# Optimization experiments

Hardware: AMD Instinct MI355X
Metric: run time of the kernel (lower is better)

The kernel has to match this reference:

```python
import jax, jax.numpy as jnp
import numpy as np

N, E = 4096, 131072
D_IN, D_H, H, D_HEAD, D_OUT, L = 768, 256, 4, 64, 128, 2


def setup_inputs() -> dict:
    key = jax.random.key(0)
    ks = jax.random.split(key, 8)
    x = jax.random.normal(ks[0], (N, D_IN), dtype=jnp.float32)
    edge_index = jax.random.randint(ks[1], (2, E), 0, N, dtype=jnp.int64)
    Win = jax.random.normal(ks[2], (D_IN, D_H), dtype=jnp.float32) * 0.02
    bin_ = jnp.zeros((D_H,), dtype=jnp.float32)
    # per-layer, per-head projection weights [L, H, D_H, D_HEAD]
    Wg = jax.random.normal(ks[3], (L, H, D_H, D_HEAD), dtype=jnp.float32) * 0.05
    # per-layer, per-head attention vectors a: [L, H, 2*D_HEAD]
    a = jax.random.normal(ks[4], (L, H, 2 * D_HEAD), dtype=jnp.float32) * 0.05
    Wout = jax.random.normal(ks[5], (D_H, D_OUT), dtype=jnp.float32) * 0.05
    bout = jnp.zeros((D_OUT,), dtype=jnp.float32)
    return {"x": x, "edge_index": edge_index, "Win": Win, "bin_": bin_,
            "Wg": Wg, "a": a, "Wout": Wout, "bout": bout}


def _gat_layer(h, Wl, al, row, col):
    # h: [N, D_H], Wl: [H, D_H, D_HEAD], al: [H, 2*D_HEAD]
    hh = jnp.einsum('ni,hio->hno', h, Wl)          # [H, N, D_HEAD]
    a_src, a_dst = al[:, :D_HEAD], al[:, D_HEAD:]
    s_src = jnp.einsum('hno,ho->hn', hh, a_src)    # [H, N]
    s_dst = jnp.einsum('hno,ho->hn', hh, a_dst)    # [H, N]
    e = jax.nn.leaky_relu(s_src[:, row] + s_dst[:, col], negative_slope=0.2)  # [H, E]
    # dense scatter exactly as the torch module: zeros then assign at (row, col)
    att = jnp.zeros((H, N, N), dtype=h.dtype).at[:, row, col].set(e)
    att = jax.nn.softmax(att, axis=-1)             # dense row softmax (zeros included)
    hp = jnp.einsum('hnm,hmo->hno', att, hh)       # [H, N, D_HEAD]
    return jnp.transpose(hp, (1, 0, 2)).reshape(N, H * D_HEAD)


def reference(x, edge_index, Win, bin_, Wg, a, Wout, bout):
    row, col = edge_index[0], edge_index[1]
    h = jax.nn.relu(x @ Win + bin_)                # input_proj + relu (dropout = eval identity)
    for l in range(L):
        h = jax.nn.relu(_gat_layer(h, Wg[l], a[l], row, col))
    node_embeddings = h @ Wout + bout              # [N, D_OUT]
    return node_embeddings
```

## Files before the change

kernel.cpp:

```cpp
#include <hip/hip_runtime.h>
#include <hip/hip_bf16.h>

#define NNODES 4096
#define NEDGES 131072
#define D_IN   768
#define D_H    256
#define NHEAD  4
#define D_HEAD 64
#define D_OUT  128
#define DEGCAP 192

typedef __attribute__((ext_vector_type(4))) float f32x4;
typedef __attribute__((ext_vector_type(8))) short bf16x8;
typedef __attribute__((ext_vector_type(8))) unsigned short u16x8;

static __device__ __forceinline__ unsigned short f2bf(float f) {
    __hip_bfloat16 h = __float2bfloat16(f);
    return *reinterpret_cast<unsigned short*>(&h);
}
static __device__ __forceinline__ float bf2f(unsigned short u) {
    return __uint_as_float((unsigned)u << 16);
}

#define OFF_H0     (0u)
#define OFF_H1     (4u<<20)
#define OFF_HH     (8u<<20)
#define OFF_SPART  (10u<<20)
#define OFF_SSRC   (OFF_SPART + 131072u)
#define OFF_SDST   (OFF_SSRC + 65536u)
#define OFF_S      (OFF_SDST + 65536u)
#define OFF_WINT   (OFF_S + 1024u)
#define OFF_WGT    (OFF_WINT + 393216u)
#define OFF_WOUTT  (OFF_WGT + 262144u)
#define OFF_BM     (OFF_WOUTT + 65536u)
#define BM_BYTES   ((size_t)NNODES*128u*4u)

__global__ __launch_bounds__(256) void zero_bm(uint4* __restrict__ bm4)
{
    bm4[blockIdx.x*256 + threadIdx.x] = make_uint4(0u,0u,0u,0u);
}

__global__ void edge_bitmap(const int* __restrict__ ei, unsigned* __restrict__ bm)
{
    __shared__ int is64_sh;
    int tid = threadIdx.x;
    if (tid < 64) {
        int v = ei[2*tid + 1];
        unsigned long long ball = __ballot(v == 0);
        if (tid == 0) is64_sh = (ball == ~0ull) ? 1 : 0;
    }
    __syncthreads();
    int is64 = is64_sh;
    int k = blockIdx.x*256 + tid;
    if (k >= NEDGES) return;
    int r = is64 ? ei[2*k]            : ei[k];
    int c = is64 ? ei[2*NEDGES + 2*k] : ei[NEDGES + k];
    r &= (NNODES-1); c &= (NNODES-1);
    atomicOr(&bm[(size_t)r*128 + (c>>5)], 1u << (c & 31));
}

__global__ __launch_bounds__(256) void convert_weights(
    const float* __restrict__ Win, const float* __restrict__ Wg,
    const float* __restrict__ Wout,
    unsigned short* __restrict__ WinT, unsigned short* __restrict__ WgT,
    unsigned short* __restrict__ WoutT)
{
    __shared__ float tile[32][33];
    int mat = blockIdx.y;
    const float* src; unsigned short* dst; int R, Cc;
    if (mat == 0)      { src = Win;                 dst = WinT;                 R = 768; Cc = 256; }
    else if (mat <= 8) { src = Wg + (size_t)(mat-1)*256*64; dst = WgT + (size_t)(mat-1)*64*256; R = 256; Cc = 64; }
    else               { src = Wout;                dst = WoutT;                R = 256; Cc = 128; }
    int tilesC = Cc >> 5;
    int tr = blockIdx.x / tilesC, tc = blockIdx.x % tilesC;
    if (tr*32 >= R) return;
    int ci = threadIdx.x & 31, rq = threadIdx.x >> 5;
    #pragma unroll
    for (int rr = rq; rr < 32; rr += 8)
        tile[rr][ci] = src[(size_t)(tr*32+rr)*Cc + tc*32 + ci];
    __syncthreads();
    int ri = threadIdx.x & 31, cq = threadIdx.x >> 5;
    #pragma unroll
    for (int cc = cq; cc < 32; cc += 8)
        dst[(size_t)(tc*32+cc)*R + tr*32 + ri] = f2bf(tile[ri][cc]);
}

__global__ __launch_bounds__(256) void gemm_mfma(
    const float* __restrict__ A, const unsigned short* __restrict__ BT,
    const float* __restrict__ bias, float* __restrict__ Cf,
    unsigned short* __restrict__ Cb,
    int M, int N, int K, int relu,
    const float* __restrict__ a_l, float* __restrict__ ssrc,
    float* __restrict__ sdst, float* __restrict__ Spart)
{
    __shared__ unsigned short As[32][72];
    __shared__ unsigned short Bs[64][72];
    __shared__ float sredS[4][32], sredD[4][32];
    const int tid = threadIdx.x;
    const int bx = blockIdx.x, by = blockIdx.y;
    const int wc = tid >> 6;
    const int lane = tid & 63;
    const int g = lane >> 4, c = lane & 15;
    const int ar = tid >> 3, ak = (tid & 7) * 8;
    const int bc = tid >> 2, bk = (tid & 3) * 16;
    f32x4 acc0 = {0.f,0.f,0.f,0.f}, acc1 = {0.f,0.f,0.f,0.f};
    const float* Arow = A + (size_t)(by*32 + ar)*K;
    const unsigned short* Brow = BT + (size_t)(bx*64 + bc)*K;

    for (int k0 = 0; k0 < K; k0 += 64) {
        float4 av0 = *(const float4*)&Arow[k0 + ak];
        float4 av1 = *(const float4*)&Arow[k0 + ak + 4];
        u16x8 bv0 = *(const u16x8*)&Brow[k0 + bk];
        u16x8 bv1 = *(const u16x8*)&Brow[k0 + bk + 8];
        ushort4 aw0, aw1;
        aw0.x = f2bf(av0.x); aw0.y = f2bf(av0.y); aw0.z = f2bf(av0.z); aw0.w = f2bf(av0.w);
        aw1.x = f2bf(av1.x); aw1.y = f2bf(av1.y); aw1.z = f2bf(av1.z); aw1.w = f2bf(av1.w);
        *(ushort4*)&As[ar][ak]     = aw0;
        *(ushort4*)&As[ar][ak + 4] = aw1;
        *(u16x8*)&Bs[bc][bk]     = bv0;
        *(u16x8*)&Bs[bc][bk + 8] = bv1;
        __syncthreads();
        bf16x8 b0  = *(bf16x8*)&Bs[wc*16 + c][g*8];
        bf16x8 b1  = *(bf16x8*)&Bs[wc*16 + c][32 + g*8];
        bf16x8 a00 = *(bf16x8*)&As[c][g*8];
        bf16x8 a01 = *(bf16x8*)&As[c][32 + g*8];
        bf16x8 a10 = *(bf16x8*)&As[16 + c][g*8];
        bf16x8 a11 = *(bf16x8*)&As[16 + c][32 + g*8];
        acc0 = __builtin_amdgcn_mfma_f32_16x16x32_bf16(a00, b0, acc0, 0, 0, 0);
        acc0 = __builtin_amdgcn_mfma_f32_16x16x32_bf16(a01, b1, acc0, 0, 0, 0);
        acc1 = __builtin_amdgcn_mfma_f32_16x16x32_bf16(a10, b0, acc1, 0, 0, 0);
        acc1 = __builtin_amdgcn_mfma_f32_16x16x32_bf16(a11, b1, acc1, 0, 0, 0);
        __syncthreads();
    }

    const int col = bx*64 + wc*16 + c;
    float bb = bias ? bias[col] : 0.f;
    #pragma unroll
    for (int t = 0; t < 2; ++t) {
        f32x4 av = t ? acc1 : acc0;
        #pragma unroll
        for (int i = 0; i < 4; ++i) {
            int r = by*32 + t*16 + g*4 + i;
            float v = av[i] + bb;
            if (relu) v = fmaxf(v, 0.f);
            if (Cb) Cb[(size_t)r*N + col] = f2bf(v);
            else    Cf[(size_t)r*N + col] = v;
        }
    }

    if (a_l) {
        int h = bx;
        float as = a_l[h*128 + wc*16 + c];
        float ad = a_l[h*128 + 64 + wc*16 + c];
        float ps[8], pd[8], cs = 0.f;
        #pragma unroll
        for (int t = 0; t < 2; ++t) {
            f32x4 av = t ? acc1 : acc0;
            #pragma unroll
            for (int i = 0; i < 4; ++i) {
                ps[t*4+i] = av[i] * as;
                pd[t*4+i] = av[i] * ad;
                cs += av[i];
            }
        }
        #pragma unroll
        for (int off = 1; off < 16; off <<= 1) {
            #pragma unroll
            for (int j = 0; j < 8; ++j) {
                ps[j] += __shfl_xor(ps[j], off);
                pd[j] += __shfl_xor(pd[j], off);
            }
        }
        if (c == 0) {
            #pragma unroll
            for (int t = 0; t < 2; ++t)
                #pragma unroll
                for (int i = 0; i < 4; ++i) {
                    sredS[wc][t*16 + g*4 + i] = ps[t*4+i];
                    sredD[wc][t*16 + g*4 + i] = pd[t*4+i];
                }
        }
        cs += __shfl_xor(cs, 16);
        cs += __shfl_xor(cs, 32);
        if (g == 0)
            Spart[by*256 + h*64 + wc*16 + c] = cs;
        __syncthreads();
        if (tid < 32) {
            float s1 = sredS[0][tid] + sredS[1][tid] + sredS[2][tid] + sredS[3][tid];
            float s2 = sredD[0][tid] + sredD[1][tid] + sredD[2][tid] + sredD[3][tid];
            int r = by*32 + tid;
            ssrc[r*4 + h] = s1;
            sdst[r*4 + h] = s2;
        }
    }
}

__global__ void colsum2(const float* __restrict__ Spart, float* __restrict__ S)
{
    int j = threadIdx.x;
    float s = 0.f;
    for (int b = 0; b < 128; ++b) s += Spart[b*256 + j];
    S[j] = s;
}

__global__ __launch_bounds__(256) void aggregate_kernel(
    const unsigned* __restrict__ bm,
    const float* __restrict__ ssrc, const float* __restrict__ sdst,
    const unsigned short* __restrict__ hh, const float* __restrict__ S,
    float* __restrict__ hout)
{
    __shared__ int   csr_lds[DEGCAP];
    __shared__ float w_lds[4*DEGCAP];
    __shared__ int   cnt_sh;
    int n = blockIdx.x;
    int tid = threadIdx.x;
    int h = tid >> 6, o = tid & 63;
    const unsigned* brow = bm + (size_t)n*128;

    if (tid < 64) {
        unsigned wA = brow[2*tid], wB = brow[2*tid + 1];
        int cpc = __popc(wA) + __popc(wB);
        int pre = cpc;
        #pragma unroll
        for (int off = 1; off < 64; off <<= 1) {
            int v = __shfl_up(pre, off);
            if (tid >= off) pre += v;
        }
        int excl = pre - cpc;
        int total = __shfl(pre, 63);
        if (total <= DEGCAP) {
            int pos = excl, base = tid*64;
            unsigned w = wA;
            while (w) { int b = __builtin_ctz(w); csr_lds[pos++] = base + b; w &= w-1; }
            w = wB; base += 32;
            while (w) { int b = __builtin_ctz(w); csr_lds[pos++] = base + b; w &= w-1; }
        }
        if (tid == 0) cnt_sh = total;
    }
    __syncthreads();
    int cnt = cnt_sh;
    float ss = ssrc[n*4 + h];

    if (cnt <= DEGCAP) {
        float mx = 0.f;
        for (int i = o; i < cnt; i += 64) {
            int m = csr_lds[i];
            float e = ss + sdst[m*4 + h];
            e = (e >= 0.f) ? e : 0.2f*e;
            mx = fmaxf(mx, e);
        }
        #pragma unroll
        for (int off = 32; off; off >>= 1) mx = fmaxf(mx, __shfl_xor(mx, off));
        float M = mx;
        float base = expf(-M);

        float zp = 0.f;
        for (int i = o; i < cnt; i += 64) {
            int m = csr_lds[i];
            float e = ss + sdst[m*4 + h];
            e = (e >= 0.f) ? e : 0.2f*e;
            float w = expf(e - M) - base;
            w_lds[h*DEGCAP + i] = w;
            zp += w;
        }
        #pragma unroll
        for (int off = 32; off; off >>= 1) zp += __shfl_xor(zp, off);

        float acc = 0.f;
        int i = 0;
        for (; i + 4 <= cnt; i += 4) {
            int m0 = csr_lds[i],   m1 = csr_lds[i+1];
            int m2 = csr_lds[i+2], m3 = csr_lds[i+3];
            float w0 = w_lds[h*DEGCAP+i],   w1 = w_lds[h*DEGCAP+i+1];
            float w2 = w_lds[h*DEGCAP+i+2], w3 = w_lds[h*DEGCAP+i+3];
            float v0 = bf2f(hh[(size_t)m0*256 + h*64 + o]);
            float v1 = bf2f(hh[(size_t)m1*256 + h*64 + o]);
            float v2 = bf2f(hh[(size_t)m2*256 + h*64 + o]);
            float v3 = bf2f(hh[(size_t)m3*256 + h*64 + o]);
            acc += w0*v0; acc += w1*v1; acc += w2*v2; acc += w3*v3;
        }
        for (; i < cnt; ++i)
            acc += w_lds[h*DEGCAP+i] * bf2f(hh[(size_t)csr_lds[i]*256 + h*64 + o]);

        float Z  = zp + (float)NNODES * base;
        float hp = (acc + base * S[h*64 + o]) / Z;
        hout[(size_t)n*256 + h*64 + o] = fmaxf(hp, 0.f);
    } else {
        float mx = 0.f;
        for (int m = o; m < NNODES; m += 64) {
            if ((brow[m>>5] >> (m & 31)) & 1u) {
                float e = ss + sdst[m*4 + h];
                e = (e >= 0.f) ? e : 0.2f*e;
                mx = fmaxf(mx, e);
            }
        }
        #pragma unroll
        for (int off = 32; off; off >>= 1) mx = fmaxf(mx, __shfl_xor(mx, off));
        float M = mx;
        float base = expf(-M);
        float zp = 0.f, acc = 0.f;
        for (int m = 0; m < NNODES; ++m) {
            if ((brow[m>>5] >> (m & 31)) & 1u) {
                float e = ss + sdst[m*4 + h];
                e = (e >= 0.f) ? e : 0.2f*e;
                float w = expf(e - M) - base;
                zp += w;
                acc += w * bf2f(hh[(size_t)m*256 + h*64 + o]);
            }
        }
        float Z  = zp + (float)NNODES * base;
        float hp = (acc + base * S[h*64 + o]) / Z;
        hout[(size_t)n*256 + h*64 + o] = fmaxf(hp, 0.f);
    }
}

static int find_size(const int* sz, int n, int want, int fallback)
{
    for (int i = 0; i < n; ++i) if (sz[i] == want) return i;
    return fallback;
}

extern "C" void kernel_launch(void* const* d_in, const int* in_sizes, int n_in,
                              void* d_out, int out_size, void* d_ws, size_t ws_size,
                              hipStream_t stream)
{
    int ix   = find_size(in_sizes, n_in, NNODES*D_IN, 0);
    int ie   = find_size(in_sizes, n_in, 2*NEDGES, 1);
    int iwin = find_size(in_sizes, n_in, D_IN*D_H, 2);
    int ibin = find_size(in_sizes, n_in, D_H, 3);
    int iwg  = find_size(in_sizes, n_in, 2*NHEAD*D_H*D_HEAD, 4);
    int ia   = find_size(in_sizes, n_in, 2*NHEAD*2*D_HEAD, 5);
    int iwo  = find_size(in_sizes, n_in, D_H*D_OUT, 6);
    int ibo  = find_size(in_sizes, n_in, D_OUT, 7);

    const float* x    = (const float*)d_in[ix];
    const int*   ei   = (const int*)d_in[ie];
    const float* Win  = (const float*)d_in[iwin];
    const float* bin_ = (const float*)d_in[ibin];
    const float* Wg   = (const float*)d_in[iwg];
    const float* a    = (const float*)d_in[ia];
    const float* Wout = (const float*)d_in[iwo];
    const float* bout = (const float*)d_in[ibo];
    float* out = (float*)d_out;

    char* ws = (char*)d_ws;
    float*          h0    = (float*)(ws + OFF_H0);
    float*          h1    = (float*)(ws + OFF_H1);
    unsigned short* hh    = (unsigned short*)(ws + OFF_HH);
    float*          Spart = (float*)(ws + OFF_SPART);
    float*          ssrc  = (float*)(ws + OFF_SSRC);
    float*          sdst  = (float*)(ws + OFF_SDST);
    float*          S     = (float*)(ws + OFF_S);
    unsigned short* WinT  = (unsigned short*)(ws + OFF_WINT);
    unsigned short* WgT   = (unsigned short*)(ws + OFF_WGT);
    unsigned short* WoutT = (unsigned short*)(ws + OFF_WOUTT);
    unsigned*       bm    = (unsigned*)(ws + OFF_BM);

    zero_bm<<<512, 256, 0, stream>>>((uint4*)bm);
    edge_bitmap<<<NEDGES/256, 256, 0, stream>>>(ei, bm);
    {
        dim3 g(192, 10);
        convert_weights<<<g, 256, 0, stream>>>(Win, Wg, Wout, WinT, WgT, WoutT);
    }

    {
        dim3 g(D_H/64, NNODES/32);
        gemm_mfma<<<g, 256, 0, stream>>>(x, WinT, bin_, h0, nullptr,
                                         NNODES, D_H, D_IN, 1,
                                         nullptr, nullptr, nullptr, nullptr);
    }

    float* hin = h0;
    float* hcur = h1;
    for (int l = 0; l < 2; ++l) {
        dim3 g2(D_H/64, NNODES/32);
        gemm_mfma<<<g2, 256, 0, stream>>>(hin, WgT + (size_t)l*NHEAD*D_HEAD*D_H,
                                          nullptr, nullptr, hh,
                                          NNODES, D_H, D_H, 0,
                                          a + (size_t)l*NHEAD*128, ssrc, sdst, Spart);
        colsum2<<<1, 256, 0, stream>>>(Spart, S);
        aggregate_kernel<<<NNODES, 256, 0, stream>>>(bm, ssrc, sdst, hh, S, hcur);
        float* t = hin; hin = hcur; hcur = t;
    }

    {
        dim3 g(D_OUT/64, NNODES/32);
        gemm_mfma<<<g, 256, 0, stream>>>(hin, WoutT, bout, out, nullptr,
                                         NNODES, D_OUT, D_H, 0,
                                         nullptr, nullptr, nullptr, nullptr);
    }
}
```

Measured before the change: 87.96 us.

## Merge prep kernels, fold column-sum into aggregation, add XCD-aware GEMM block mapping

```diff
diff --git a/kernel.cpp b/kernel.cpp
--- a/kernel.cpp
+++ b/kernel.cpp
@@ -9,6 +9,10 @@
 #define D_HEAD 64
 #define D_OUT  128
 #define DEGCAP 192
+#define CONV_WIN  196608
+#define CONV_WG   131072
+#define CONV_WOUT 32768
+#define CONV_TOTAL (CONV_WIN + CONV_WG + CONV_WOUT)
 
 typedef __attribute__((ext_vector_type(4))) float f32x4;
 typedef __attribute__((ext_vector_type(8))) short bf16x8;
@@ -28,76 +32,75 @@
 #define OFF_SPART  (10u<<20)
 #define OFF_SSRC   (OFF_SPART + 131072u)
 #define OFF_SDST   (OFF_SSRC + 65536u)
-#define OFF_S      (OFF_SDST + 65536u)
-#define OFF_WINT   (OFF_S + 1024u)
+#define OFF_WINT   (OFF_SDST + 65536u)
 #define OFF_WGT    (OFF_WINT + 393216u)
 #define OFF_WOUTT  (OFF_WGT + 262144u)
 #define OFF_BM     (OFF_WOUTT + 65536u)
-#define BM_BYTES   ((size_t)NNODES*128u*4u)
-
-__global__ __launch_bounds__(256) void zero_bm(uint4* __restrict__ bm4)
+
+struct GemmShared {
+    unsigned short As[32][72];
+    unsigned short Bs[64][72];
+    float sredS[4][32];
+    float sredD[4][32];
+};
+
+__global__ __launch_bounds__(256) void k_zero_bm(uint4* __restrict__ bm4)
 {
     bm4[blockIdx.x*256 + threadIdx.x] = make_uint4(0u,0u,0u,0u);
 }
 
-__global__ void edge_bitmap(const int* __restrict__ ei, unsigned* __restrict__ bm)
-{
-    __shared__ int is64_sh;
-    int tid = threadIdx.x;
+__global__ __launch_bounds__(256) void k_prep(
+    const int* __restrict__ ei, unsigned* __restrict__ bm,
+    const float* __restrict__ Win, const float* __restrict__ Wg,
+    const float* __restrict__ Wout,
+    unsigned short* __restrict__ WinT, unsigned short* __restrict__ WgT,
+    unsigned short* __restrict__ WoutT)
+{
+    __shared__ int flag;
+    int tid = threadIdx.x, bid = blockIdx.x;
     if (tid < 64) {
         int v = ei[2*tid + 1];
         unsigned long long ball = __ballot(v == 0);
-        if (tid == 0) is64_sh = (ball == ~0ull) ? 1 : 0;
+        if (tid == 0) flag = (ball == ~0ull) ? 1 : 0;
     }
     __syncthreads();
-    int is64 = is64_sh;
-    int k = blockIdx.x*256 + tid;
-    if (k >= NEDGES) return;
+    int is64 = flag;
+    int k = bid*256 + tid;
     int r = is64 ? ei[2*k]            : ei[k];
     int c = is64 ? ei[2*NEDGES + 2*k] : ei[NEDGES + k];
     r &= (NNODES-1); c &= (NNODES-1);
     atomicOr(&bm[(size_t)r*128 + (c>>5)], 1u << (c & 31));
-}
-
-__global__ __launch_bounds__(256) void convert_weights(
-    const float* __restrict__ Win, const float* __restrict__ Wg,
-    const float* __restrict__ Wout,
-    unsigned short* __restrict__ WinT, unsigned short* __restrict__ WgT,
-    unsigned short* __restrict__ WoutT)
-{
-    __shared__ float tile[32][33];
-    int mat = blockIdx.y;
-    const float* src; unsigned short* dst; int R, Cc;
-    if (mat == 0)      { src = Win;                 dst = WinT;                 R = 768; Cc = 256; }
-    else if (mat <= 8) { src = Wg + (size_t)(mat-1)*256*64; dst = WgT + (size_t)(mat-1)*64*256; R = 256; Cc = 64; }
-    else               { src = Wout;                dst = WoutT;                R = 256; Cc = 128; }
-    int tilesC = Cc >> 5;
-    int tr = blockIdx.x / tilesC, tc = blockIdx.x % tilesC;
-    if (tr*32 >= R) return;
-    int ci = threadIdx.x & 31, rq = threadIdx.x >> 5;
-    #pragma unroll
-    for (int rr = rq; rr < 32; rr += 8)
-        tile[rr][ci] = src[(size_t)(tr*32+rr)*Cc + tc*32 + ci];
-    __syncthreads();
-    int ri = threadIdx.x & 31, cq = threadIdx.x >> 5;
-    #pragma unroll
-    for (int cc = cq; cc < 32; cc += 8)
-        dst[(size_t)(tc*32+cc)*R + tr*32 + ri] = f2bf(tile[ri][cc]);
-}
-
-__global__ __launch_bounds__(256) void gemm_mfma(
+
+    for (int d = bid*256 + tid; d < CONV_TOTAL; d += 512*256) {
+        if (d < CONV_WIN) {
+            int cc = d / 768, kk = d - cc*768;
+            WinT[d] = f2bf(Win[(size_t)kk*256 + cc]);
+        } else if (d < CONV_WIN + CONV_WG) {
+            int e = d - CONV_WIN;
+            int m = e >> 14, rem = e & 16383;
+            int o = rem >> 8, i = rem & 255;
+            WgT[e] = f2bf(Wg[(size_t)m*16384 + i*64 + o]);
+        } else {
+            int e = d - (CONV_WIN + CONV_WG);
+            int cc = e >> 8, kk = e & 255;
+            WoutT[e] = f2bf(Wout[(size_t)kk*128 + cc]);
+        }
+    }
+}
+
+__global__ __launch_bounds__(256) void k_gemm(
     const float* __restrict__ A, const unsigned short* __restrict__ BT,
     const float* __restrict__ bias, float* __restrict__ Cf,
-    unsigned short* __restrict__ Cb,
-    int M, int N, int K, int relu,
+    unsigned short* __restrict__ Cb, int N, int K, int relu, int nbx,
     const float* __restrict__ a_l, float* __restrict__ ssrc,
     float* __restrict__ sdst, float* __restrict__ Spart)
 {
-    __shared__ unsigned short As[32][72];
-    __shared__ unsigned short Bs[64][72];
-    __shared__ float sredS[4][32], sredD[4][32];
+    __shared__ GemmShared sm;
+    const int bid = blockIdx.x;
+    const int xcd = bid & 7, q = bid >> 3;
+    const int bx = q % nbx;
+    const int by = (q / nbx)*8 + xcd;
     const int tid = threadIdx.x;
-    const int bx = blockIdx.x, by = blockIdx.y;
     const int wc = tid >> 6;
     const int lane = tid & 63;
     const int g = lane >> 4, c = lane & 15;
@@ -115,17 +118,17 @@
         ushort4 aw0, aw1;
         aw0.x = f2bf(av0.x); aw0.y = f2bf(av0.y); aw0.z = f2bf(av0.z); aw0.w = f2bf(av0.w);
         aw1.x = f2bf(av1.x); aw1.y = f2bf(av1.y); aw1.z = f2bf(av1.z); aw1.w = f2bf(av1.w);
-        *(ushort4*)&As[ar][ak]     = aw0;
-        *(ushort4*)&As[ar][ak + 4] = aw1;
-        *(u16x8*)&Bs[bc][bk]     = bv0;
-        *(u16x8*)&Bs[bc][bk + 8] = bv1;
-        __syncthreads();
-        bf16x8 b0  = *(bf16x8*)&Bs[wc*16 + c][g*8];
-        bf16x8 b1  = *(bf16x8*)&Bs[wc*16 + c][32 + g*8];
-        bf16x8 a00 = *(bf16x8*)&As[c][g*8];
-        bf16x8 a01 = *(bf16x8*)&As[c][32 + g*8];
-        bf16x8 a10 = *(bf16x8*)&As[16 + c][g*8];
-        bf16x8 a11 = *(bf16x8*)&As[16 + c][32 + g*8];
+        *(ushort4*)&sm.As[ar][ak]     = aw0;
+        *(ushort4*)&sm.As[ar][ak + 4] = aw1;
+        *(u16x8*)&sm.Bs[bc][bk]     = bv0;
+        *(u16x8*)&sm.Bs[bc][bk + 8] = bv1;
+        __syncthreads();
+        bf16x8 b0  = *(bf16x8*)&sm.Bs[wc*16 + c][g*8];
+        bf16x8 b1  = *(bf16x8*)&sm.Bs[wc*16 + c][32 + g*8];
+        bf16x8 a00 = *(bf16x8*)&sm.As[c][g*8];
+        bf16x8 a01 = *(bf16x8*)&sm.As[c][32 + g*8];
+        bf16x8 a10 = *(bf16x8*)&sm.As[16 + c][g*8];
+        bf16x8 a11 = *(bf16x8*)&sm.As[16 + c][32 + g*8];
         acc0 = __builtin_amdgcn_mfma_f32_16x16x32_bf16(a00, b0, acc0, 0, 0, 0);
         acc0 = __builtin_amdgcn_mfma_f32_16x16x32_bf16(a01, b1, acc0, 0, 0, 0);
         acc1 = __builtin_amdgcn_mfma_f32_16x16x32_bf16(a10, b0, acc1, 0, 0, 0);
@@ -176,18 +179,18 @@
             for (int t = 0; t < 2; ++t)
                 #pragma unroll
                 for (int i = 0; i < 4; ++i) {
-                    sredS[wc][t*16 + g*4 + i] = ps[t*4+i];
-                    sredD[wc][t*16 + g*4 + i] = pd[t*4+i];
+                    sm.sredS[wc][t*16 + g*4 + i] = ps[t*4+i];
+                    sm.sredD[wc][t*16 + g*4 + i] = pd[t*4+i];
                 }
         }
         cs += __shfl_xor(cs, 16);
         cs += __shfl_xor(cs, 32);
         if (g == 0)
-            Spart[by*256 + h*64 + wc*16 + c] = cs;
+            Spart[by*256 + col] = cs;
         __syncthreads();
         if (tid < 32) {
-            float s1 = sredS[0][tid] + sredS[1][tid] + sredS[2][tid] + sredS[3][tid];
-            float s2 = sredD[0][tid] + sredD[1][tid] + sredD[2][tid] + sredD[3][tid];
+            float s1 = sm.sredS[0][tid] + sm.sredS[1][tid] + sm.sredS[2][tid] + sm.sredS[3][tid];
+            float s2 = sm.sredD[0][tid] + sm.sredD[1][tid] + sm.sredD[2][tid] + sm.sredD[3][tid];
             int r = by*32 + tid;
             ssrc[r*4 + h] = s1;
             sdst[r*4 + h] = s2;
@@ -195,122 +198,120 @@
     }
 }
 
-__global__ void colsum2(const float* __restrict__ Spart, float* __restrict__ S)
-{
-    int j = threadIdx.x;
-    float s = 0.f;
-    for (int b = 0; b < 128; ++b) s += Spart[b*256 + j];
-    S[j] = s;
-}
-
-__global__ __launch_bounds__(256) void aggregate_kernel(
-    const unsigned* __restrict__ bm,
-    const float* __restrict__ ssrc, const float* __restrict__ sdst,
-    const unsigned short* __restrict__ hh, const float* __restrict__ S,
-    float* __restrict__ hout)
-{
-    __shared__ int   csr_lds[DEGCAP];
-    __shared__ float w_lds[4*DEGCAP];
+__global__ __launch_bounds__(256) void k_agg(
+    const unsigned* __restrict__ bm, const float* __restrict__ ssrc,
+    const float* __restrict__ sdst, const unsigned short* __restrict__ hh,
+    const float* __restrict__ Spart, float* __restrict__ hout)
+{
+    __shared__ int   csr[DEGCAP];
+    __shared__ float wl[4*DEGCAP];
     __shared__ int   cnt_sh;
-    int n = blockIdx.x;
-    int tid = threadIdx.x;
-    int h = tid >> 6, o = tid & 63;
-    const unsigned* brow = bm + (size_t)n*128;
-
-    if (tid < 64) {
-        unsigned wA = brow[2*tid], wB = brow[2*tid + 1];
-        int cpc = __popc(wA) + __popc(wB);
-        int pre = cpc;
-        #pragma unroll
-        for (int off = 1; off < 64; off <<= 1) {
-            int v = __shfl_up(pre, off);
-            if (tid >= off) pre += v;
-        }
-        int excl = pre - cpc;
-        int total = __shfl(pre, 63);
-        if (total <= DEGCAP) {
-            int pos = excl, base = tid*64;
-            unsigned w = wA;
-            while (w) { int b = __builtin_ctz(w); csr_lds[pos++] = base + b; w &= w-1; }
-            w = wB; base += 32;
-            while (w) { int b = __builtin_ctz(w); csr_lds[pos++] = base + b; w &= w-1; }
-        }
-        if (tid == 0) cnt_sh = total;
-    }
-    __syncthreads();
-    int cnt = cnt_sh;
-    float ss = ssrc[n*4 + h];
-
-    if (cnt <= DEGCAP) {
-        float mx = 0.f;
-        for (int i = o; i < cnt; i += 64) {
-            int m = csr_lds[i];
-            float e = ss + sdst[m*4 + h];
-            e = (e >= 0.f) ? e : 0.2f*e;
-            mx = fmaxf(mx, e);
-        }
-        #pragma unroll
-        for (int off = 32; off; off >>= 1) mx = fmaxf(mx, __shfl_xor(mx, off));
-        float M = mx;
-        float base = expf(-M);
-
-        float zp = 0.f;
-        for (int i = o; i < cnt; i += 64) {
-            int m = csr_lds[i];
-            float e = ss + sdst[m*4 + h];
-            e = (e >= 0.f) ? e : 0.2f*e;
-            float w = expf(e - M) - base;
-            w_lds[h*DEGCAP + i] = w;
-            zp += w;
-        }
-        #pragma unroll
-        for (int off = 32; off; off >>= 1) zp += __shfl_xor(zp, off);
-
-        float acc = 0.f;
-        int i = 0;
-        for (; i + 4 <= cnt; i += 4) {
-            int m0 = csr_lds[i],   m1 = csr_lds[i+1];
-            int m2 = csr_lds[i+2], m3 = csr_lds[i+3];
-            float w0 = w_lds[h*DEGCAP+i],   w1 = w_lds[h*DEGCAP+i+1];
-            float w2 = w_lds[h*DEGCAP+i+2], w3 = w_lds[h*DEGCAP+i+3];
-            float v0 = bf2f(hh[(size_t)m0*256 + h*64 + o]);
-            float v1 = bf2f(hh[(size_t)m1*256 + h*64 + o]);
-            float v2 = bf2f(hh[(size_t)m2*256 + h*64 + o]);
-            float v3 = bf2f(hh[(size_t)m3*256 + h*64 + o]);
-            acc += w0*v0; acc += w1*v1; acc += w2*v2; acc += w3*v3;
-        }
-        for (; i < cnt; ++i)
-            acc += w_lds[h*DEGCAP+i] * bf2f(hh[(size_t)csr_lds[i]*256 + h*64 + o]);
-
-        float Z  = zp + (float)NNODES * base;
-        float hp = (acc + base * S[h*64 + o]) / Z;
-        hout[(size_t)n*256 + h*64 + o] = fmaxf(hp, 0.f);
-    } else {
-        float mx = 0.f;
-        for (int m = o; m < NNODES; m += 64) {
-            if ((brow[m>>5] >> (m & 31)) & 1u) {
+    const int tid = threadIdx.x;
+    const int h = tid >> 6, o = tid & 63;
+
+    float Sv = 0.f;
+    for (int b = 0; b < 128; ++b) Sv += Spart[b*256 + tid];
+
+    for (int v = 0; v < 4; ++v) {
+        int n = v*1024 + blockIdx.x;
+        const unsigned* brow = bm + (size_t)n*128;
+
+        if (tid < 64) {
+            unsigned wA = brow[2*tid], wB = brow[2*tid + 1];
+            int cpc = __popc(wA) + __popc(wB);
+            int pre = cpc;
+            #pragma unroll
+            for (int off = 1; off < 64; off <<= 1) {
+                int vv = __shfl_up(pre, off);
+                if (tid >= off) pre += vv;
+            }
+            int excl = pre - cpc;
+            int total = __shfl(pre, 63);
+            if (total <= DEGCAP) {
+                int pos = excl, base = tid*64;
+                unsigned w = wA;
+                while (w) { int b = __builtin_ctz(w); csr[pos++] = base + b; w &= w-1; }
+                w = wB; base += 32;
+                while (w) { int b = __builtin_ctz(w); csr[pos++] = base + b; w &= w-1; }
+            }
+            if (tid == 0) cnt_sh = total;
+        }
+        __syncthreads();
+        int cnt = cnt_sh;
+        float ss = ssrc[n*4 + h];
+
+        if (cnt <= DEGCAP) {
+            float mx = 0.f;
+            for (int i = o; i < cnt; i += 64) {
+                int m = csr[i];
                 float e = ss + sdst[m*4 + h];
                 e = (e >= 0.f) ? e : 0.2f*e;
                 mx = fmaxf(mx, e);
             }
-        }
-        #pragma unroll
-        for (int off = 32; off; off >>= 1) mx = fmaxf(mx, __shfl_xor(mx, off));
-        float M = mx;
-        float base = expf(-M);
-        float zp = 0.f, acc = 0.f;
-        for (int m = 0; m < NNODES; ++m) {
-            if ((brow[m>>5] >> (m & 31)) & 1u) {
+            #pragma unroll
+            for (int off = 32; off; off >>= 1) mx = fmaxf(mx, __shfl_xor(mx, off));
+            float M = mx;
+            float base = expf(-M);
+
+            float zp = 0.f;
+            for (int i = o; i < cnt; i += 64) {
+                int m = csr[i];
                 float e = ss + sdst[m*4 + h];
                 e = (e >= 0.f) ? e : 0.2f*e;
                 float w = expf(e - M) - base;
+                wl[h*DEGCAP + i] = w;
                 zp += w;
-                acc += w * bf2f(hh[(size_t)m*256 + h*64 + o]);
-            }
-        }
-        float Z  = zp + (float)NNODES * base;
-        float hp = (acc + base * S[h*64 + o]) / Z;
-        hout[(size_t)n*256 + h*64 + o] = fmaxf(hp, 0.f);
+            }
+            #pragma unroll
+            for (int off = 32; off; off >>= 1) zp += __shfl_xor(zp, off);
+
+            float acc = 0.f;
+            int i = 0;
+            for (; i + 4 <= cnt; i += 4) {
+                int m0 = csr[i],   m1 = csr[i+1];
+                int m2 = csr[i+2], m3 = csr[i+3];
+                float w0 = wl[h*DEGCAP+i],   w1 = wl[h*DEGCAP+i+1];
+                float w2 = wl[h*DEGCAP+i+2], w3 = wl[h*DEGCAP+i+3];
+                float v0 = bf2f(hh[(size_t)m0*256 + h*64 + o]);
+                float v1 = bf2f(hh[(size_t)m1*256 + h*64 + o]);
+                float v2 = bf2f(hh[(size_t)m2*256 + h*64 + o]);
+                float v3 = bf2f(hh[(size_t)m3*256 + h*64 + o]);
+                acc += w0*v0; acc += w1*v1; acc += w2*v2; acc += w3*v3;
+            }
+            for (; i < cnt; ++i)
+                acc += wl[h*DEGCAP+i] * bf2f(hh[(size_t)csr[i]*256 + h*64 + o]);
+
+            float Z  = zp + (float)NNODES * base;
+            float hp = (acc + base * Sv) / Z;
+            hout[(size_t)n*256 + tid] = fmaxf(hp, 0.f);
+        } else {
+            float mx = 0.f;
+            for (int m = o; m < NNODES; m += 64) {
+                if ((brow[m>>5] >> (m & 31)) & 1u) {
+                    float e = ss + sdst[m*4 + h];
+                    e = (e >= 0.f) ? e : 0.2f*e;
+                    mx = fmaxf(mx, e);
+                }
+            }
+            #pragma unroll
+            for (int off = 32; off; off >>= 1) mx = fmaxf(mx, __shfl_xor(mx, off));
+            float M = mx;
+            float base = expf(-M);
+            float zp = 0.f, acc = 0.f;
+            for (int m = 0; m < NNODES; ++m) {
+                if ((brow[m>>5] >> (m & 31)) & 1u) {
+                    float e = ss + sdst[m*4 + h];
+                    e = (e >= 0.f) ? e : 0.2f*e;
+                    float w = expf(e - M) - base;
+                    zp += w;
+                    acc += w * bf2f(hh[(size_t)m*256 + h*64 + o]);
+                }
+            }
+            float Z  = zp + (float)NNODES * base;
+            float hp = (acc + base * Sv) / Z;
+            hout[(size_t)n*256 + tid] = fmaxf(hp, 0.f);
+        }
+        __syncthreads();
     }
 }
 
@@ -350,43 +351,27 @@
     float*          Spart = (float*)(ws + OFF_SPART);
     float*          ssrc  = (float*)(ws + OFF_SSRC);
     float*          sdst  = (float*)(ws + OFF_SDST);
-    float*          S     = (float*)(ws + OFF_S);
     unsigned short* WinT  = (unsigned short*)(ws + OFF_WINT);
     unsigned short* WgT   = (unsigned short*)(ws + OFF_WGT);
     unsigned short* WoutT = (unsigned short*)(ws + OFF_WOUTT);
     unsigned*       bm    = (unsigned*)(ws + OFF_BM);
 
-    zero_bm<<<512, 256, 0, stream>>>((uint4*)bm);
-    edge_bitmap<<<NEDGES/256, 256, 0, stream>>>(ei, bm);
-    {
-        dim3 g(192, 10);
-        convert_weights<<<g, 256, 0, stream>>>(Win, Wg, Wout, WinT, WgT, WoutT);
-    }
-
-    {
-        dim3 g(D_H/64, NNODES/32);
-        gemm_mfma<<<g, 256, 0, stream>>>(x, WinT, bin_, h0, nullptr,
-                                         NNODES, D_H, D_IN, 1,
-                                         nullptr, nullptr, nullptr, nullptr);
-    }
+    k_zero_bm<<<512, 256, 0, stream>>>((uint4*)bm);
+    k_prep<<<512, 256, 0, stream>>>(ei, bm, Win, Wg, Wout, WinT, WgT, WoutT);
+
+    k_gemm<<<512, 256, 0, stream>>>(x, WinT, bin_, h0, nullptr, D_H, D_IN, 1, 4,
+                                    nullptr, nullptr, nullptr, nullptr);
 
     float* hin = h0;
     float* hcur = h1;
     for (int l = 0; l < 2; ++l) {
-        dim3 g2(D_H/64, NNODES/32);
-        gemm_mfma<<<g2, 256, 0, stream>>>(hin, WgT + (size_t)l*NHEAD*D_HEAD*D_H,
-                                          nullptr, nullptr, hh,
-                                          NNODES, D_H, D_H, 0,
-                                          a + (size_t)l*NHEAD*128, ssrc, sdst, Spart);
-        colsum2<<<1, 256, 0, stream>>>(Spart, S);
-        aggregate_kernel<<<NNODES, 256, 0, stream>>>(bm, ssrc, sdst, hh, S, hcur);
+        k_gemm<<<512, 256, 0, stream>>>(hin, WgT + (size_t)l*NHEAD*D_HEAD*D_H,
+                                        nullptr, nullptr, hh, D_H, D_H, 0, 4,
+                                        a + (size_t)l*NHEAD*128, ssrc, sdst, Spart);
+        k_agg<<<1024, 256, 0, stream>>>(bm, ssrc, sdst, hh, Spart, hcur);
         float* t = hin; hin = hcur; hcur = t;
     }
 
-    {
-        dim3 g(D_OUT/64, NNODES/32);
-        gemm_mfma<<<g, 256, 0, stream>>>(hin, WoutT, bout, out, nullptr,
-                                         NNODES, D_OUT, D_H, 0,
-                                         nullptr, nullptr, nullptr, nullptr);
-    }
-}
+    k_gemm<<<256, 256, 0, stream>>>(hin, WoutT, bout, out, nullptr, D_OUT, D_H, 0, 2,
+                                    nullptr, nullptr, nullptr, nullptr);
+}
```

New measurement: 105.6 us. 1.2x slower.
